# Performance work log

Hardware: AMD Instinct MI355X
Metric: run time of the kernel (lower is better)

Reference implementation:

```python
import jax, jax.numpy as jnp
import numpy as np

B, N, H, D, T = 2, 512, 128, 128, 8  # batch, nodes, feat width, mid/out size, triplet fts
Z = 2 * H  # concat(node_fts, hidden)


def _lin_params(key, fan_in, fan_out):
    kw, kb = jax.random.split(key)
    scale = 1.0 / np.sqrt(fan_in)
    w = jax.random.uniform(kw, (fan_in, fan_out), jnp.float32, -scale, scale)
    b = jax.random.uniform(kb, (fan_out,), jnp.float32, -scale, scale)
    return w, b


def setup_inputs() -> dict:
    key = jax.random.key(0)
    ks = jax.random.split(key, 16)
    inp = {
        'node_fts': jax.random.normal(ks[0], (B, N, H), jnp.float32),
        'edge_fts': jax.random.normal(ks[1], (B, N, N, H), jnp.float32),
        'graph_fts': jax.random.normal(ks[2], (B, H), jnp.float32),
        'adj_mat': (jax.random.uniform(ks[3], (B, N, N)) < 0.5).astype(jnp.float32),
        'hidden': jax.random.normal(ks[4], (B, N, H), jnp.float32),
    }
    # message linears
    inp['Wm1'], inp['bm1'] = _lin_params(ks[5], Z, D)
    inp['Wm2'], inp['bm2'] = _lin_params(ks[6], Z, D)
    inp['Wme'], inp['bme'] = _lin_params(ks[7], H, D)
    inp['Wmg'], inp['bmg'] = _lin_params(ks[8], H, D)
    # output linears
    inp['Wo1'], inp['bo1'] = _lin_params(ks[9], Z, D)
    inp['Wo2'], inp['bo2'] = _lin_params(ks[10], D, D)
    # triplet linears
    inp['Wt1'], inp['bt1'] = _lin_params(ks[11], Z, T)
    inp['Wt2'], inp['bt2'] = _lin_params(ks[12], Z, T)
    inp['Wte'], inp['bte'] = _lin_params(ks[13], H, T)
    inp['Wtg'], inp['btg'] = _lin_params(ks[14], H, T)
    return inp


def reference(node_fts, edge_fts, graph_fts, adj_mat, hidden,
              Wm1, bm1, Wm2, bm2, Wme, bme, Wmg, bmg,
              Wo1, bo1, Wo2, bo2,
              Wt1, bt1, Wt2, bt2, Wte, bte, Wtg, btg):
    z = jnp.concatenate([node_fts, hidden], axis=-1)  # [b,n,2h]

    msg_1 = z @ Wm1 + bm1            # [b,n,d]
    msg_2 = z @ Wm2 + bm2            # [b,n,d]
    msg_e = edge_fts @ Wme + bme     # [b,n,n,d]
    msg_g = graph_fts @ Wmg + bmg    # [b,d]

    # triplet messages: broadcast pairwise sum -> relu, shape [b,n,n,t]
    tri = (z @ Wt1 + bt1)[:, None, :, :] \
        + (z @ Wt2 + bt2)[:, :, None, :] \
        + (edge_fts @ Wte + bte) \
        + (graph_fts @ Wtg + btg)[:, None, None, :]
    tri_msgs = jax.nn.relu(tri)

    # pairwise message broadcast-add, mask by adjacency, max over senders (axis 1)
    msgs = msg_1[:, None, :, :] + msg_2[:, :, None, :] + msg_e \
         + msg_g[:, None, None, :]                      # [b,n,n,d]
    msgs = jnp.max(msgs * adj_mat[..., None], axis=1)   # [b,n,d]

    ret = (z @ Wo1 + bo1) + (msgs @ Wo2 + bo2)           # [b,n,d]
    return (ret, tri_msgs)
```

## Files before the change

kernel.cpp:

```cpp
#include <hip/hip_runtime.h>
#include <hip/hip_bf16.h>

#define NB 2
#define NN 512
#define HH 128
#define DD 128
#define TT 8

#define WPACK_OFF 0
#define C_OFF     36864
#define BROW_OFF  561152
#define TC_OFF    1085440
#define TB_OFF    1118208
#define OC_OFF    1150976
#define PART_OFF  1675264
#define ZF_OFF    10063872

#define OUT_TRI   131072

#define AP 132

typedef float f32x4 __attribute__((ext_vector_type(4)));
typedef short s16x8 __attribute__((ext_vector_type(8)));

__device__ __forceinline__ unsigned short f2bf(float f) {
    union { float f; unsigned int u; } x; x.f = f;
    unsigned int u = x.u;
    unsigned int r = (u + 0x7FFFu + ((u >> 16) & 1u)) >> 16;
    return (unsigned short)r;
}

__device__ __forceinline__ unsigned cvt2bf(float a, float b) {
#if __has_builtin(__builtin_amdgcn_cvt_pk_bf16_f32)
    auto r = __builtin_amdgcn_cvt_pk_bf16_f32(a, b);
    return __builtin_bit_cast(unsigned, r);
#else
    return (unsigned)f2bf(a) | ((unsigned)f2bf(b) << 16);
#endif
}

__global__ __launch_bounds__(256) void k0_precompute(
    const float* __restrict__ node, const float* __restrict__ hidden,
    const float* __restrict__ graph,
    const float* __restrict__ Wm1, const float* __restrict__ Wm2,
    const float* __restrict__ Wo1, const float* __restrict__ Wmg,
    const float* __restrict__ Wt1, const float* __restrict__ Wt2,
    const float* __restrict__ Wtg,
    const float* __restrict__ Wme, const float* __restrict__ Wte,
    const float* __restrict__ bm1, const float* __restrict__ bm2,
    const float* __restrict__ bme, const float* __restrict__ bmg,
    const float* __restrict__ bo1, const float* __restrict__ bo2,
    const float* __restrict__ bt1, const float* __restrict__ bt2,
    const float* __restrict__ bte, const float* __restrict__ btg,
    char* __restrict__ ws)
{
    const int bx = blockIdx.x, tid = threadIdx.x;
    if (bx == 512) {
        unsigned short* wp = (unsigned short*)(ws + WPACK_OFF);
        for (int idx = tid; idx < 16 * 144 * 8; idx += 256) {
            int j = idx & 7, tmp = idx >> 3;
            int n = tmp % 144, kq = tmp / 144;
            int k = kq * 8 + j;
            float v = 0.f;
            if (n < 128) v = Wme[k * 128 + n];
            else if (n < 136) v = Wte[k * 8 + (n - 128)];
            wp[idx] = f2bf(v);
        }
        return;
    }
    __shared__ float zs[2 * 260];
    const int row0 = bx * 2;
    const int b = row0 >> 9;
    #pragma unroll
    for (int e = 0; e < 2; e++) {
        int idx = e * 256 + tid;
        int rl = idx >> 8, col = idx & 255;
        float v = (col < 128) ? node[(row0 + rl) * 128 + col]
                              : hidden[(row0 + rl) * 128 + col - 128];
        zs[rl * 260 + col] = v;
    }
    __syncthreads();

    float* Cws = (float*)(ws + C_OFF);
    float* Bws = (float*)(ws + BROW_OFF);
    float* Ows = (float*)(ws + OC_OFF);
    float* TCw = (float*)(ws + TC_OFF);
    float* TBw = (float*)(ws + TB_OFF);

    const int d = tid & 127, half = tid >> 7;
    const int row = row0 + half;
    const float* z = zs + half * 260;
    float c = 0.f, q = 0.f, o = 0.f;
    #pragma unroll 8
    for (int k = 0; k < 256; k++) {
        float za = z[k];
        c = fmaf(za, Wm1[k * 128 + d], c);
        q = fmaf(za, Wm2[k * 128 + d], q);
        o = fmaf(za, Wo1[k * 128 + d], o);
    }
    float gm = 0.f;
    #pragma unroll 8
    for (int k = 0; k < 128; k++) gm = fmaf(graph[b * 128 + k], Wmg[k * 128 + d], gm);
    const float cb = gm + bm1[d] + bm2[d] + bme[d] + bmg[d];
    Cws[row * 128 + d] = c + cb;
    Bws[row * 128 + d] = q;
    Ows[row * 128 + d] = o + bo1[d] + bo2[d];

    if (tid < 32) {
        int rl = tid >> 4, t = (tid >> 1) & 7, which = tid & 1;
        const float* zr = zs + rl * 260;
        const float* W = which ? Wt2 : Wt1;
        float acc = 0.f;
        #pragma unroll 8
        for (int k = 0; k < 256; k++) acc = fmaf(zr[k], W[k * 8 + t], acc);
        int rg = row0 + rl;
        if (which == 0) {
            float gt = 0.f;
            #pragma unroll 8
            for (int k = 0; k < 128; k++) gt = fmaf(graph[b * 128 + k], Wtg[k * 8 + t], gt);
            TCw[rg * 8 + t] = acc + gt + bt1[t] + bt2[t] + bte[t] + btg[t];
        } else {
            TBw[rg * 8 + t] = acc;
        }
    }
}

__global__ __launch_bounds__(256, 4) void k2_main(
    const float* __restrict__ edge, const float* __restrict__ adj,
    char* __restrict__ ws, float* __restrict__ out)
{
    __shared__ __align__(16) float As[2][16 * AP];
    const int tid = threadIdx.x;
    const int jt = blockIdx.x, ic = blockIdx.y, b = blockIdx.z;
    const int j0 = jt * 16, i0 = ic * 32;

    const int lane = tid & 63, wave = tid >> 6;
    const int quad = lane >> 4, l15 = lane & 15;

    const float* Bws = (const float*)(ws + BROW_OFF);
    const float* TCw = (const float*)(ws + TC_OFF);
    const float* TBw = (const float*)(ws + TB_OFF);
    const s16x8* wp8 = (const s16x8*)(ws + WPACK_OFF);
    float* part = (float*)(ws + PART_OFF);
    int* Zws = (int*)(ws + ZF_OFF);

    s16x8 Bf[2][4], Bt[4];
    #pragma unroll
    for (int s = 0; s < 4; s++) {
        Bf[0][s] = wp8[(4 * s + quad) * 144 + (2 * wave) * 16 + l15];
        Bf[1][s] = wp8[(4 * s + quad) * 144 + (2 * wave + 1) * 16 + l15];
        Bt[s]    = wp8[(4 * s + quad) * 144 + 128 + l15];
    }

    const int jb = j0 + quad * 4;
    float TCf[4];
    #pragma unroll
    for (int r = 0; r < 4; r++)
        TCf[r] = (l15 < 8) ? TCw[(b * 512 + jb + r) * 8 + l15] : 0.f;

    const int f0 = tid, f1 = tid + 256;
    const int g0off = (f0 >> 5) * 128 + (f0 & 31) * 4;
    const int g1off = (f1 >> 5) * 128 + (f1 & 31) * 4;
    const int l0off = (f0 >> 5) * AP + (f0 & 31) * 4;
    const int l1off = (f1 >> 5) * AP + (f1 & 31) * 4;

    const size_t ebase = ((size_t)(b * 512 + i0) * 512 + j0) * 128;
    {
        const float* nb = edge + ebase;
        *(float4*)&As[0][l0off] = *(const float4*)(nb + g0off);
        *(float4*)&As[0][l1off] = *(const float4*)(nb + g1off);
    }
    __syncthreads();

    float Mx[2][4];
    #pragma unroll
    for (int ntl = 0; ntl < 2; ntl++)
        #pragma unroll
        for (int r = 0; r < 4; r++) Mx[ntl][r] = -INFINITY;
    int anyz[4] = {0, 0, 0, 0};

    const int c0 = (2 * wave) * 16 + l15, c1 = c0 + 16;

    for (int ii = 0; ii < 32; ii++) {
        const int p = ii & 1, pn = p ^ 1;
        const int ig = i0 + ii;
        const int rowb = b * 512 + ig;

        float4 st0, st1;
        if (ii < 31) {
            const float* nb = edge + ebase + (size_t)(ii + 1) * 65536;
            st0 = *(const float4*)(nb + g0off);
            st1 = *(const float4*)(nb + g1off);
        }
        const float4 adjv = *(const float4*)(adj + (size_t)rowb * 512 + jb);
        const float brw0 = Bws[rowb * 128 + c0];
        const float brw1 = Bws[rowb * 128 + c1];
        const float tb   = TBw[rowb * 8 + (l15 & 7)];

        s16x8 af[4];
        const float* ap = &As[p][l15 * AP + quad * 8];
        #pragma unroll
        for (int s = 0; s < 4; s++) {
            float4 pv = *(const float4*)(ap + s * 32);
            float4 qv = *(const float4*)(ap + s * 32 + 4);
            union { s16x8 v; unsigned u[4]; } pk;
            pk.u[0] = cvt2bf(pv.x, pv.y);
            pk.u[1] = cvt2bf(pv.z, pv.w);
            pk.u[2] = cvt2bf(qv.x, qv.y);
            pk.u[3] = cvt2bf(qv.z, qv.w);
            af[s] = pk.v;
        }

        f32x4 acc0 = (f32x4){0.f, 0.f, 0.f, 0.f};
        f32x4 acc1 = (f32x4){0.f, 0.f, 0.f, 0.f};
        #pragma unroll
        for (int s = 0; s < 4; s++) {
            acc0 = __builtin_amdgcn_mfma_f32_16x16x32_bf16(af[s], Bf[0][s], acc0, 0, 0, 0);
            acc1 = __builtin_amdgcn_mfma_f32_16x16x32_bf16(af[s], Bf[1][s], acc1, 0, 0, 0);
        }
        const int trimine = ((ii & 3) == wave);
        f32x4 acct = (f32x4){0.f, 0.f, 0.f, 0.f};
        if (trimine) {
            #pragma unroll
            for (int s = 0; s < 4; s++)
                acct = __builtin_amdgcn_mfma_f32_16x16x32_bf16(af[s], Bt[s], acct, 0, 0, 0);
        }

        if (ii < 31) {
            *(float4*)&As[pn][l0off] = st0;
            *(float4*)&As[pn][l1off] = st1;
        }

        const float av[4] = {adjv.x, adjv.y, adjv.z, adjv.w};
        #pragma unroll
        for (int r = 0; r < 4; r++) {
            const int isz = (av[r] == 0.f);
            anyz[r] |= isz;
            Mx[0][r] = fmaxf(Mx[0][r], isz ? -INFINITY : (acc0[r] + brw0));
            Mx[1][r] = fmaxf(Mx[1][r], isz ? -INFINITY : (acc1[r] + brw1));
        }
        if (trimine && l15 < 8) {
            float* tout = out + OUT_TRI + ((size_t)rowb * 512 + jb) * 8 + l15;
            #pragma unroll
            for (int r = 0; r < 4; r++)
                tout[r * 8] = fmaxf(acct[r] + TCf[r] + tb, 0.f);
        }
        __syncthreads();
    }

    #pragma unroll
    for (int r = 0; r < 4; r++) {
        const size_t pb = ((size_t)(b * 16 + ic) * 512 + jb + r) * 128;
        part[pb + c0] = Mx[0][r];
        part[pb + c1] = Mx[1][r];
    }
    if (wave == 0 && l15 == 0) {
        #pragma unroll
        for (int r = 0; r < 4; r++)
            Zws[(b * 16 + ic) * 512 + jb + r] = anyz[r];
    }
}

__global__ __launch_bounds__(128) void k3_final(
    const char* __restrict__ ws, const float* __restrict__ Wo2,
    float* __restrict__ out)
{
    __shared__ float ms[128];
    const int bj = blockIdx.x, d = threadIdx.x;
    const int b = bj >> 9, j = bj & 511;
    const float* part = (const float*)(ws + PART_OFF);
    const int* Zws = (const int*)(ws + ZF_OFF);
    const float* Cws = (const float*)(ws + C_OFF);
    const float* Ows = (const float*)(ws + OC_OFF);

    const int rj = b * 512 + j;
    float m = -INFINITY;
    int zf = 0;
    #pragma unroll
    for (int ic = 0; ic < 16; ic++) {
        m = fmaxf(m, part[((size_t)(b * 16 + ic) * 512 + j) * 128 + d]);
        zf |= Zws[(b * 16 + ic) * 512 + j];
    }
    float c = Cws[rj * 128 + d];
    float mm = fmaxf(m + c, zf ? 0.f : -INFINITY);
    ms[d] = mm;
    __syncthreads();
    float acc = Ows[rj * 128 + d];
    #pragma unroll 8
    for (int k = 0; k < 128; k++) acc = fmaf(ms[k], Wo2[k * 128 + d], acc);
    out[rj * 128 + d] = acc;
}

extern "C" void kernel_launch(void* const* d_in, const int* in_sizes, int n_in,
                              void* d_out, int out_size, void* d_ws, size_t ws_size,
                              hipStream_t stream) {
    const float* node   = (const float*)d_in[0];
    const float* edge   = (const float*)d_in[1];
    const float* graph  = (const float*)d_in[2];
    const float* adj    = (const float*)d_in[3];
    const float* hidden = (const float*)d_in[4];
    const float* Wm1 = (const float*)d_in[5];  const float* bm1 = (const float*)d_in[6];
    const float* Wm2 = (const float*)d_in[7];  const float* bm2 = (const float*)d_in[8];
    const float* Wme = (const float*)d_in[9];  const float* bme = (const float*)d_in[10];
    const float* Wmg = (const float*)d_in[11]; const float* bmg = (const float*)d_in[12];
    const float* Wo1 = (const float*)d_in[13]; const float* bo1 = (const float*)d_in[14];
    const float* Wo2 = (const float*)d_in[15]; const float* bo2 = (const float*)d_in[16];
    const float* Wt1 = (const float*)d_in[17]; const float* bt1 = (const float*)d_in[18];
    const float* Wt2 = (const float*)d_in[19]; const float* bt2 = (const float*)d_in[20];
    const float* Wte = (const float*)d_in[21]; const float* bte = (const float*)d_in[22];
    const float* Wtg = (const float*)d_in[23]; const float* btg = (const float*)d_in[24];
    float* out = (float*)d_out;
    char* ws = (char*)d_ws;

    k0_precompute<<<dim3(513), dim3(256), 0, stream>>>(
        node, hidden, graph, Wm1, Wm2, Wo1, Wmg, Wt1, Wt2, Wtg, Wme, Wte,
        bm1, bm2, bme, bmg, bo1, bo2, bt1, bt2, bte, btg, ws);
    k2_main<<<dim3(32, 16, 2), dim3(256), 0, stream>>>(edge, adj, ws, out);
    k3_final<<<dim3(1024), dim3(128), 0, stream>>>(ws, Wo2, out);
}
```

Before: 470.8 us.

## Stream edge tiles directly into LDS with async loads and deeper buffering

Replaces the register-staged double buffer for edge tiles with global_load_lds direct-to-LDS copies into a 4-deep ring, prefetching two rows ahead and synchronising through explicit vmcnt waits and barriers. The padded LDS layout gives way to an XOR-swizzled layout so the fragment reads avoid bank conflicts. The goal is to hide more global-load latency and cut the register and VGPR-to-LDS store traffic in the memory-bound main loop. The triplet stores also move ahead of the max update. The hand-counted vmcnt values are fragile: the extra adj, Bws and TBw loads and the triplet stores share the counter, which risks both over-waiting and correctness hazards.

```diff
diff --git a/kernel.cpp b/kernel.cpp
--- a/kernel.cpp
+++ b/kernel.cpp
@@ -18,8 +18,6 @@
 
 #define OUT_TRI   131072
 
-#define AP 132
-
 typedef float f32x4 __attribute__((ext_vector_type(4)));
 typedef short s16x8 __attribute__((ext_vector_type(8)));
 
@@ -37,6 +35,13 @@
 #else
     return (unsigned)f2bf(a) | ((unsigned)f2bf(b) << 16);
 #endif
+}
+
+__device__ __forceinline__ void glds16(const float* g, void* l) {
+    __builtin_amdgcn_global_load_lds(
+        (const __attribute__((address_space(1))) unsigned int*)g,
+        (__attribute__((address_space(3))) unsigned int*)l,
+        16, 0, 0);
 }
 
 __global__ __launch_bounds__(256) void k0_precompute(
@@ -129,7 +134,7 @@
     const float* __restrict__ edge, const float* __restrict__ adj,
     char* __restrict__ ws, float* __restrict__ out)
 {
-    __shared__ __align__(16) float As[2][16 * AP];
+    __shared__ __align__(16) float As[4][2048];
     const int tid = threadIdx.x;
     const int jt = blockIdx.x, ic = blockIdx.y, b = blockIdx.z;
     const int j0 = jt * 16, i0 = ic * 32;
@@ -158,19 +163,21 @@
     for (int r = 0; r < 4; r++)
         TCf[r] = (l15 < 8) ? TCw[(b * 512 + jb + r) * 8 + l15] : 0.f;
 
-    const int f0 = tid, f1 = tid + 256;
-    const int g0off = (f0 >> 5) * 128 + (f0 & 31) * 4;
-    const int g1off = (f1 >> 5) * 128 + (f1 & 31) * 4;
-    const int l0off = (f0 >> 5) * AP + (f0 & 31) * 4;
-    const int l1off = (f1 >> 5) * AP + (f1 & 31) * 4;
+    const int r0 = tid >> 5;
+    const int g0 = r0 * 128 + (((tid & 31) ^ (r0 & 7)) << 2);
+    const int g1 = g0 + 1024;
+    const int lw = (tid & ~63) << 4;
 
     const size_t ebase = ((size_t)(b * 512 + i0) * 512 + j0) * 128;
+
     {
-        const float* nb = edge + ebase;
-        *(float4*)&As[0][l0off] = *(const float4*)(nb + g0off);
-        *(float4*)&As[0][l1off] = *(const float4*)(nb + g1off);
-    }
-    __syncthreads();
+        const float* s0p = edge + ebase;
+        const float* s1p = edge + ebase + 65536;
+        glds16(s0p + g0, (char*)As + lw);
+        glds16(s0p + g1, (char*)As + 4096 + lw);
+        glds16(s1p + g0, (char*)As + 8192 + lw);
+        glds16(s1p + g1, (char*)As + 8192 + 4096 + lw);
+    }
 
     float Mx[2][4];
     #pragma unroll
@@ -180,29 +187,38 @@
     int anyz[4] = {0, 0, 0, 0};
 
     const int c0 = (2 * wave) * 16 + l15, c1 = c0 + 16;
+    const int e0 = (2 * quad) ^ (l15 & 7);
 
     for (int ii = 0; ii < 32; ii++) {
-        const int p = ii & 1, pn = p ^ 1;
+        if (ii == 0)      asm volatile("s_waitcnt vmcnt(2)" ::: "memory");
+        else if (ii < 31) asm volatile("s_waitcnt vmcnt(6)" ::: "memory");
+        else              asm volatile("s_waitcnt vmcnt(0)" ::: "memory");
+        __builtin_amdgcn_s_barrier();
+
         const int ig = i0 + ii;
         const int rowb = b * 512 + ig;
 
-        float4 st0, st1;
-        if (ii < 31) {
-            const float* nb = edge + ebase + (size_t)(ii + 1) * 65536;
-            st0 = *(const float4*)(nb + g0off);
-            st1 = *(const float4*)(nb + g1off);
-        }
         const float4 adjv = *(const float4*)(adj + (size_t)rowb * 512 + jb);
         const float brw0 = Bws[rowb * 128 + c0];
         const float brw1 = Bws[rowb * 128 + c1];
         const float tb   = TBw[rowb * 8 + (l15 & 7)];
-
+        __builtin_amdgcn_sched_barrier(0);
+
+        if (ii < 30) {
+            const float* sp = edge + ebase + (size_t)(ii + 2) * 65536;
+            char* lb = (char*)As + ((ii + 2) & 3) * 8192;
+            glds16(sp + g0, lb + lw);
+            glds16(sp + g1, lb + 4096 + lw);
+        }
+
+        const float* bufp = &As[ii & 3][0];
+        const float* pA = bufp + l15 * 128 + e0 * 4;
+        const float* pB = bufp + l15 * 128 + (e0 ^ 1) * 4;
         s16x8 af[4];
-        const float* ap = &As[p][l15 * AP + quad * 8];
         #pragma unroll
         for (int s = 0; s < 4; s++) {
-            float4 pv = *(const float4*)(ap + s * 32);
-            float4 qv = *(const float4*)(ap + s * 32 + 4);
+            float4 pv = *(const float4*)(pA + s * 32);
+            float4 qv = *(const float4*)(pB + s * 32);
             union { s16x8 v; unsigned u[4]; } pk;
             pk.u[0] = cvt2bf(pv.x, pv.y);
             pk.u[1] = cvt2bf(pv.z, pv.w);
@@ -226,9 +242,11 @@
                 acct = __builtin_amdgcn_mfma_f32_16x16x32_bf16(af[s], Bt[s], acct, 0, 0, 0);
         }
 
-        if (ii < 31) {
-            *(float4*)&As[pn][l0off] = st0;
-            *(float4*)&As[pn][l1off] = st1;
+        if (trimine && l15 < 8) {
+            float* tout = out + OUT_TRI + ((size_t)rowb * 512 + jb) * 8 + l15;
+            #pragma unroll
+            for (int r = 0; r < 4; r++)
+                tout[r * 8] = fmaxf(acct[r] + TCf[r] + tb, 0.f);
         }
 
         const float av[4] = {adjv.x, adjv.y, adjv.z, adjv.w};
@@ -239,13 +257,6 @@
             Mx[0][r] = fmaxf(Mx[0][r], isz ? -INFINITY : (acc0[r] + brw0));
             Mx[1][r] = fmaxf(Mx[1][r], isz ? -INFINITY : (acc1[r] + brw1));
         }
-        if (trimine && l15 < 8) {
-            float* tout = out + OUT_TRI + ((size_t)rowb * 512 + jb) * 8 + l15;
-            #pragma unroll
-            for (int r = 0; r < 4; r++)
-                tout[r * 8] = fmaxf(acct[r] + TCf[r] + tb, 0.f);
-        }
-        __syncthreads();
     }
 
     #pragma unroll
```

Result: slower. 481.0 us (+2.2%).

## Load edge tile fragments directly into registers, dropping LDS staging and barriers

Applied to the files above, without the earlier changes.

The main kernel no longer stages each 16x128 edge slice through a double-buffered shared-memory tile. Each lane now loads its MFMA A-fragment straight from global memory into registers and prefetches the next row one iteration ahead, which removes the per-iteration __syncthreads and LDS round trip. The cost is more register pressure (occupancy hint lowered from 4 to 3 blocks per CU). Every wave also loads the full tile redundantly, which multiplies global/L2 read traffic by four compared with the cooperative load.

```diff
diff --git a/kernel.cpp b/kernel.cpp
--- a/kernel.cpp
+++ b/kernel.cpp
@@ -17,8 +17,6 @@
 #define ZF_OFF    10063872
 
 #define OUT_TRI   131072
-
-#define AP 132
 
 typedef float f32x4 __attribute__((ext_vector_type(4)));
 typedef short s16x8 __attribute__((ext_vector_type(8)));
@@ -125,11 +123,10 @@
     }
 }
 
-__global__ __launch_bounds__(256, 4) void k2_main(
+__global__ __launch_bounds__(256, 3) void k2_main(
     const float* __restrict__ edge, const float* __restrict__ adj,
     char* __restrict__ ws, float* __restrict__ out)
 {
-    __shared__ __align__(16) float As[2][16 * AP];
     const int tid = threadIdx.x;
     const int jt = blockIdx.x, ic = blockIdx.y, b = blockIdx.z;
     const int j0 = jt * 16, i0 = ic * 32;
@@ -158,19 +155,8 @@
     for (int r = 0; r < 4; r++)
         TCf[r] = (l15 < 8) ? TCw[(b * 512 + jb + r) * 8 + l15] : 0.f;
 
-    const int f0 = tid, f1 = tid + 256;
-    const int g0off = (f0 >> 5) * 128 + (f0 & 31) * 4;
-    const int g1off = (f1 >> 5) * 128 + (f1 & 31) * 4;
-    const int l0off = (f0 >> 5) * AP + (f0 & 31) * 4;
-    const int l1off = (f1 >> 5) * AP + (f1 & 31) * 4;
-
-    const size_t ebase = ((size_t)(b * 512 + i0) * 512 + j0) * 128;
-    {
-        const float* nb = edge + ebase;
-        *(float4*)&As[0][l0off] = *(const float4*)(nb + g0off);
-        *(float4*)&As[0][l1off] = *(const float4*)(nb + g1off);
-    }
-    __syncthreads();
+    const float* gA = edge + ((size_t)(b * 512 + i0) * 512 + (j0 + l15)) * 128
+                    + quad * 8;
 
     float Mx[2][4];
     #pragma unroll
@@ -181,35 +167,42 @@
 
     const int c0 = (2 * wave) * 16 + l15, c1 = c0 + 16;
 
+    float4 pf[8];
+    #pragma unroll
+    for (int s = 0; s < 4; s++) {
+        pf[2 * s]     = *(const float4*)(gA + s * 32);
+        pf[2 * s + 1] = *(const float4*)(gA + s * 32 + 4);
+    }
+    const float* gp = gA + 65536;
+
     for (int ii = 0; ii < 32; ii++) {
-        const int p = ii & 1, pn = p ^ 1;
         const int ig = i0 + ii;
         const int rowb = b * 512 + ig;
 
-        float4 st0, st1;
+        s16x8 af[4];
+        #pragma unroll
+        for (int s = 0; s < 4; s++) {
+            union { s16x8 v; unsigned u[4]; } pk;
+            pk.u[0] = cvt2bf(pf[2 * s].x, pf[2 * s].y);
+            pk.u[1] = cvt2bf(pf[2 * s].z, pf[2 * s].w);
+            pk.u[2] = cvt2bf(pf[2 * s + 1].x, pf[2 * s + 1].y);
+            pk.u[3] = cvt2bf(pf[2 * s + 1].z, pf[2 * s + 1].w);
+            af[s] = pk.v;
+        }
+
         if (ii < 31) {
-            const float* nb = edge + ebase + (size_t)(ii + 1) * 65536;
-            st0 = *(const float4*)(nb + g0off);
-            st1 = *(const float4*)(nb + g1off);
-        }
+            #pragma unroll
+            for (int s = 0; s < 4; s++) {
+                pf[2 * s]     = *(const float4*)(gp + s * 32);
+                pf[2 * s + 1] = *(const float4*)(gp + s * 32 + 4);
+            }
+            gp += 65536;
+        }
+
         const float4 adjv = *(const float4*)(adj + (size_t)rowb * 512 + jb);
         const float brw0 = Bws[rowb * 128 + c0];
         const float brw1 = Bws[rowb * 128 + c1];
         const float tb   = TBw[rowb * 8 + (l15 & 7)];
-
-        s16x8 af[4];
-        const float* ap = &As[p][l15 * AP + quad * 8];
-        #pragma unroll
-        for (int s = 0; s < 4; s++) {
-            float4 pv = *(const float4*)(ap + s * 32);
-            float4 qv = *(const float4*)(ap + s * 32 + 4);
-            union { s16x8 v; unsigned u[4]; } pk;
-            pk.u[0] = cvt2bf(pv.x, pv.y);
-            pk.u[1] = cvt2bf(pv.z, pv.w);
-            pk.u[2] = cvt2bf(qv.x, qv.y);
-            pk.u[3] = cvt2bf(qv.z, qv.w);
-            af[s] = pk.v;
-        }
 
         f32x4 acc0 = (f32x4){0.f, 0.f, 0.f, 0.f};
         f32x4 acc1 = (f32x4){0.f, 0.f, 0.f, 0.f};
@@ -226,9 +219,11 @@
                 acct = __builtin_amdgcn_mfma_f32_16x16x32_bf16(af[s], Bt[s], acct, 0, 0, 0);
         }
 
-        if (ii < 31) {
-            *(float4*)&As[pn][l0off] = st0;
-            *(float4*)&As[pn][l1off] = st1;
+        if (trimine && l15 < 8) {
+            float* tout = out + OUT_TRI + ((size_t)rowb * 512 + jb) * 8 + l15;
+            #pragma unroll
+            for (int r = 0; r < 4; r++)
+                tout[r * 8] = fmaxf(acct[r] + TCf[r] + tb, 0.f);
         }
 
         const float av[4] = {adjv.x, adjv.y, adjv.z, adjv.w};
@@ -239,13 +234,6 @@
             Mx[0][r] = fmaxf(Mx[0][r], isz ? -INFINITY : (acc0[r] + brw0));
             Mx[1][r] = fmaxf(Mx[1][r], isz ? -INFINITY : (acc1[r] + brw1));
         }
-        if (trimine && l15 < 8) {
-            float* tout = out + OUT_TRI + ((size_t)rowb * 512 + jb) * 8 + l15;
-            #pragma unroll
-            for (int r = 0; r < 4; r++)
-                tout[r * 8] = fmaxf(acct[r] + TCf[r] + tb, 0.f);
-        }
-        __syncthreads();
     }
 
     #pragma unroll
```

Measured after the change: 524.1 us. 1.11x slower.
